# Optimization experiments

Measured on AMD Instinct MI355X. Metric: run time of the kernel, lower is better.

Reference implementation:

```python
import jax, jax.numpy as jnp
import numpy as np
import math

N = 12288
IN_MAIN, IN_MOD = 64, 128
NC_INNER, NC_QK, OUT_MAIN = 16, 8, 64

def setup_inputs() -> dict:
    key = jax.random.key(0)
    ks = jax.random.split(key, 8)
    s = lambda fan_in: 1.0 / np.sqrt(fan_in)
    return {
        "x_main": jax.random.normal(ks[0], (N, IN_MAIN), dtype=jnp.float32),
        "x_mod": jax.random.normal(ks[1], (N, IN_MOD), dtype=jnp.float32),
        "xyz": jax.random.uniform(ks[2], (N, 3), dtype=jnp.float32),
        # MLP E: [in_main+in_mod -> nc_inner -> nc_inner], bias=False (weights stored [in, out])
        "W_e1": jax.random.uniform(ks[3], (IN_MAIN + IN_MOD, NC_INNER), jnp.float32, -s(IN_MAIN + IN_MOD), s(IN_MAIN + IN_MOD)),
        "W_e2": jax.random.uniform(ks[4], (NC_INNER, NC_INNER), jnp.float32, -s(NC_INNER), s(NC_INNER)),
        "W_q": jax.random.uniform(ks[5], (NC_INNER, NC_QK), jnp.float32, -s(NC_INNER), s(NC_INNER)),
        "W_k": jax.random.uniform(ks[6], (NC_INNER, NC_QK), jnp.float32, -s(NC_INNER), s(NC_INNER)),
        "W_v": jax.random.uniform(ks[7], (NC_INNER, OUT_MAIN), jnp.float32, -s(NC_INNER), s(NC_INNER)),
    }

def reference(x_main, x_mod, xyz, W_e1, W_e2, W_q, W_k, W_v):
    # concat 3D + 2D features: [N, in_main+in_mod]
    x = jnp.concatenate((x_main, x_mod), axis=-1)
    # MLP E (bias-free Linear + ReLU per layer): [N, nc_inner]
    h = jax.nn.relu(jax.nn.relu(x @ W_e1) @ W_e2)
    Q = h @ W_q  # [N, nc_qk]
    K = h @ W_k  # [N, nc_qk]
    V = h @ W_v  # [N, out_main]
    scale = 1.0 / math.sqrt(NC_QK)
    scores = (Q @ K.T) * scale          # [N, N] full global attention
    attn = jax.nn.softmax(scores, axis=1)
    return attn @ V                     # [N, out_main]
```

## Files before the change

### kernel.cpp

```cpp
#include <hip/hip_runtime.h>
#include <stdint.h>


#define NN 12288

typedef float    f32x16 __attribute__((ext_vector_type(16)));
typedef short    s16x8  __attribute__((ext_vector_type(8)));
typedef unsigned short u16;

#define MFMA_32x32x16_BF16 __builtin_amdgcn_mfma_f32_32x32x16_bf16

#define OFF_QB   0u
#define OFF_VT   196608u
#define OFF_PO   2162688u

__device__ __forceinline__ float bf2f(u16 s) {
    union { unsigned int u; float f; } c; c.u = ((unsigned int)s) << 16; return c.f;
}
__device__ __forceinline__ u16 f2bf(float f) {
    union { float f; unsigned int u; } c; c.f = f;
    return (u16)((c.u + 0x8000u) >> 16);
}
__device__ __forceinline__ unsigned int pk2(float a, float b) {
    union { float f; unsigned int u; } ca, cb; ca.f = a; cb.f = b;
    return ((ca.u + 0x8000u) >> 16) | ((cb.u + 0x8000u) & 0xffff0000u);
}
__device__ __forceinline__ unsigned int pkbf(float a, float b) {
#if __has_builtin(__builtin_amdgcn_cvt_pk_bf16_f32)
    auto r = __builtin_amdgcn_cvt_pk_bf16_f32(a, b);
    union { decltype(r) v; unsigned int u; } c; c.v = r; return c.u;
#else
    return pk2(a, b);
#endif
}
__device__ __forceinline__ f32x16 zf16() {
    f32x16 z;
#pragma unroll
    for (int i = 0; i < 16; ++i) z[i] = 0.f;
    return z;
}
__device__ __forceinline__ s16x8 zs8() {
    s16x8 z;
#pragma unroll
    for (int i = 0; i < 8; ++i) z[i] = 0;
    return z;
}

union U8 { s16x8 v; unsigned int u[4]; };
union QV { uint4 q; s16x8 v; };

__global__ __launch_bounds__(256) void k1_qkv(
    const void* __restrict__ xmain, const void* __restrict__ xmod,
    const void* __restrict__ we1, const void* __restrict__ we2,
    const void* __restrict__ wqp, const void* __restrict__ wkp,
    const void* __restrict__ wvp,
    u16* __restrict__ qb, u16* __restrict__ vt)
{
    __shared__ float wf[4608];
    __shared__ int   sflag;
    __shared__ float lh1[64][4][17];
    __shared__ float lh2[64][17];

    const int t = threadIdx.x;
    const int r = t >> 2;
    const int p = t & 3;
    const int row = blockIdx.x * 64 + r;

    if (t == 0) sflag = 0;
    __syncthreads();
    {
        float v = bf2f(((const u16*)xmod)[2 * t]);
        if (fabsf(v) > 16.f) atomicAdd(&sflag, 1);
    }
    __syncthreads();
    const int isf32 = (sflag > 8);

    const float SCL = 0.51006979f;
    if (isf32) {
        const float* a1 = (const float*)we1; const float* a2 = (const float*)we2;
        const float* aq = (const float*)wqp; const float* ak = (const float*)wkp;
        const float* av = (const float*)wvp;
        for (int i = t; i < 4608; i += 256) {
            if      (i < 3072) wf[i] = a1[i];
            else if (i < 3328) wf[i] = a2[i - 3072];
            else if (i < 3456) wf[i] = aq[i - 3328] * SCL;
            else if (i < 3584) wf[i] = ak[i - 3456];
            else               wf[i] = av[i - 3584];
        }
    } else {
        const u16* a1 = (const u16*)we1; const u16* a2 = (const u16*)we2;
        const u16* aq = (const u16*)wqp; const u16* ak = (const u16*)wkp;
        const u16* av = (const u16*)wvp;
        for (int i = t; i < 4608; i += 256) {
            if      (i < 3072) wf[i] = bf2f(a1[i]);
            else if (i < 3328) wf[i] = bf2f(a2[i - 3072]);
            else if (i < 3456) wf[i] = bf2f(aq[i - 3328]) * SCL;
            else if (i < 3584) wf[i] = bf2f(ak[i - 3456]);
            else               wf[i] = bf2f(av[i - 3584]);
        }
    }
    __syncthreads();

    const float* __restrict__ W1 = wf;
    const float* __restrict__ W2 = wf + 3072;
    const float* __restrict__ Wq = wf + 3328;
    const float* __restrict__ Wk = wf + 3456;
    const float* __restrict__ Wv = wf + 3584;

    float h1p[16];
#pragma unroll
    for (int o = 0; o < 16; ++o) h1p[o] = 0.f;

    if (isf32) {
#pragma unroll
        for (int cc = 0; cc < 12; ++cc) {
            const int c = p + cc * 4;
            float4 xv = (c < 16)
                ? ((const float4*)xmain)[(size_t)row * 16 + c]
                : ((const float4*)xmod)[(size_t)row * 32 + (c - 16)];
            float xs[4] = {xv.x, xv.y, xv.z, xv.w};
#pragma unroll
            for (int j = 0; j < 4; ++j) {
                const float* wr = W1 + (c * 4 + j) * 16;
#pragma unroll
                for (int o = 0; o < 16; ++o) h1p[o] += xs[j] * wr[o];
            }
        }
    } else {
#pragma unroll
        for (int cc = 0; cc < 12; ++cc) {
            const int c = p + cc * 4;
            uint2 xv = (c < 16)
                ? ((const uint2*)xmain)[(size_t)row * 16 + c]
                : ((const uint2*)xmod)[(size_t)row * 32 + (c - 16)];
            float xs[4] = { bf2f((u16)(xv.x & 0xffff)), bf2f((u16)(xv.x >> 16)),
                            bf2f((u16)(xv.y & 0xffff)), bf2f((u16)(xv.y >> 16)) };
#pragma unroll
            for (int j = 0; j < 4; ++j) {
                const float* wr = W1 + (c * 4 + j) * 16;
#pragma unroll
                for (int o = 0; o < 16; ++o) h1p[o] += xs[j] * wr[o];
            }
        }
    }
#pragma unroll
    for (int o = 0; o < 16; ++o) lh1[r][p][o] = h1p[o];
    __syncthreads();

    float h1[16];
#pragma unroll
    for (int o = 0; o < 16; ++o)
        h1[o] = fmaxf(lh1[r][0][o] + lh1[r][1][o] + lh1[r][2][o] + lh1[r][3][o], 0.f);

#pragma unroll
    for (int oo = 0; oo < 4; ++oo) {
        const int o = p * 4 + oo;
        float s = 0.f;
#pragma unroll
        for (int j = 0; j < 16; ++j) s += h1[j] * W2[j * 16 + o];
        lh2[r][o] = fmaxf(s, 0.f);
    }
    __syncthreads();

    float h2[16];
#pragma unroll
    for (int j = 0; j < 16; ++j) h2[j] = lh2[r][j];

    {
        float q0 = 0.f, q1 = 0.f, k0 = 0.f, k1 = 0.f;
        const int o = 2 * p;
#pragma unroll
        for (int j = 0; j < 16; ++j) {
            q0 += h2[j] * Wq[j * 8 + o];
            q1 += h2[j] * Wq[j * 8 + o + 1];
            k0 += h2[j] * Wk[j * 8 + o];
            k1 += h2[j] * Wk[j * 8 + o + 1];
        }
        ((unsigned int*)qb)[(size_t)row * 4 + p] = pk2(q0, q1);
        ((unsigned int*)vt)[(size_t)(row >> 6) * 2304 + 2048 +
                            (row & 63) * 4 + p] = pk2(k0, k1);
    }

    {
        const int ch = row >> 6, tI = (row >> 5) & 1, kk = row & 31;
        const int b   = kk >> 4, kk4 = kk & 15;
        const int hh  = (kk4 >> 2) & 1;
        const int jj  = (kk4 & 3) + 4 * (kk4 >> 3);
        const size_t cbase = (size_t)ch * 4608 + (size_t)(tI * 4 + b) * 512
                           + hh * 256 + jj;
#pragma unroll
        for (int c16 = 0; c16 < 16; ++c16) {
            const int c = p * 16 + c16;
            float v = 0.f;
#pragma unroll
            for (int j = 0; j < 16; ++j) v += h2[j] * Wv[j * 64 + c];
            vt[cbase + (size_t)(c >> 5) * 1024 + (c & 31) * 8] = f2bf(v);
        }
    }
}


__global__ __launch_bounds__(256, 3) void k2_attn(
    const u16* __restrict__ qb, const u16* __restrict__ vt,
    u16* __restrict__ po, float* __restrict__ pl,
    int nsplit, int ntile)
{
    __shared__ float sf[4][2178];

    const int tid  = threadIdx.x;
    const int lane = tid & 63;
    const int half = lane >> 5;
    const int l31  = lane & 31;
    const int w    = tid >> 6;
    const int qB   = (blockIdx.x % 96) * 128;
    const int sp   = blockIdx.x / 96;
    const int myq  = qB + 32 * w;
    const int key_start = sp * (NN / nsplit);
    const char* vbase = (const char*)vt + (size_t)(key_start >> 6) * 9216;

    const f32x16 Z = zf16();
    s16x8 qf = zs8();
    if (!half) qf = *(const s16x8*)(qb + (size_t)(myq + l31) * 8);

    s16x8 ones;
#pragma unroll
    for (int i = 0; i < 8; ++i) ones[i] = (short)0x3F80;

    f32x16 acc0 = Z, acc1 = Z, accl = Z;

    QV kaA, f00A, f10A, f01A, f11A;
    QV kaB, f00B, f10B, f01B, f11B;

#define LDT(gt, ka, f00, f10, f01, f11) do {                                  \
    const char* cb_ = vbase + (size_t)((gt) >> 1) * 9216 + ((gt) & 1) * 4096; \
    (f00).q = *(const uint4*)(cb_ +        lane * 16);                        \
    (f01).q = *(const uint4*)(cb_ + 1024 + lane * 16);                        \
    (f10).q = *(const uint4*)(cb_ + 2048 + lane * 16);                        \
    (f11).q = *(const uint4*)(cb_ + 3072 + lane * 16);                        \
    (ka).q  = *(const uint4*)(vbase + (size_t)((gt) >> 1) * 9216 + 8192       \
                              + ((gt) & 1) * 512 + l31 * 16);                 \
} while (0)

#define TILE(ka, f00, f10, f01, f11) do {                                     \
    f32x16 S_ = MFMA_32x32x16_BF16((ka).v, qf, Z, 0, 0, 0);                   \
    float pr_[16];                                                            \
    _Pragma("unroll")                                                         \
    for (int r_ = 0; r_ < 16; ++r_) pr_[r_] = __builtin_amdgcn_exp2f(S_[r_]); \
    U8 p0_, p1_;                                                              \
    _Pragma("unroll")                                                         \
    for (int i_ = 0; i_ < 4; ++i_) {                                          \
        p0_.u[i_] = pkbf(pr_[2 * i_],     pr_[2 * i_ + 1]);                   \
        p1_.u[i_] = pkbf(pr_[8 + 2 * i_], pr_[8 + 2 * i_ + 1]);               \
    }                                                                         \
    accl = MFMA_32x32x16_BF16(ones, p0_.v, accl, 0, 0, 0);                    \
    accl = MFMA_32x32x16_BF16(ones, p1_.v, accl, 0, 0, 0);                    \
    acc0 = MFMA_32x32x16_BF16((f00).v, p0_.v, acc0, 0, 0, 0);                 \
    acc1 = MFMA_32x32x16_BF16((f10).v, p0_.v, acc1, 0, 0, 0);                 \
    acc0 = MFMA_32x32x16_BF16((f01).v, p1_.v, acc0, 0, 0, 0);                 \
    acc1 = MFMA_32x32x16_BF16((f11).v, p1_.v, acc1, 0, 0, 0);                 \
} while (0)

    LDT(0, kaA, f00A, f10A, f01A, f11A);
    int gt = 0;
    for (; gt + 2 < ntile; gt += 2) {
        LDT(gt + 1, kaB, f00B, f10B, f01B, f11B);
        TILE(kaA, f00A, f10A, f01A, f11A);
        LDT(gt + 2, kaA, f00A, f10A, f01A, f11A);
        TILE(kaB, f00B, f10B, f01B, f11B);
    }
    LDT(gt + 1, kaB, f00B, f10B, f01B, f11B);
    TILE(kaA, f00A, f10A, f01A, f11A);
    TILE(kaB, f00B, f10B, f01B, f11B);

#undef LDT
#undef TILE

    const float ls = accl[0];

    float* sfw = &sf[w][0];
#pragma unroll
    for (int r = 0; r < 16; ++r) {
        const int c = (r & 3) + 8 * (r >> 2) + 4 * half;
        sfw[c * 33 + l31]        = acc0[r];
        sfw[(32 + c) * 33 + l31] = acc1[r];
    }
    if (lane < 32) sfw[2112 + l31] = ls;

    u16* poS = po + (size_t)sp * (NN * 64);
    const int lq  = lane >> 1;
    const int cb0 = (lane & 1) * 32;
    unsigned int u[16];
#pragma unroll
    for (int i = 0; i < 16; ++i)
        u[i] = pkbf(sfw[(cb0 + 2 * i) * 33 + lq],
                    sfw[(cb0 + 2 * i + 1) * 33 + lq]);
    u16* dst = poS + (size_t)(myq + lq) * 64 + cb0;
    *(uint4*)(dst)      = make_uint4(u[0],  u[1],  u[2],  u[3]);
    *(uint4*)(dst + 8)  = make_uint4(u[4],  u[5],  u[6],  u[7]);
    *(uint4*)(dst + 16) = make_uint4(u[8],  u[9],  u[10], u[11]);
    *(uint4*)(dst + 24) = make_uint4(u[12], u[13], u[14], u[15]);
    if (lane < 32)
        pl[(size_t)sp * NN + myq + l31] = sfw[2112 + l31];
}

__global__ __launch_bounds__(256) void k3_norm(
    const u16* __restrict__ po, const float* __restrict__ pl,
    float4* __restrict__ out, int nsplit)
{
    const int i = blockIdx.x * 256 + threadIdx.x;
    const int row = i >> 4;
    const int c0 = (i & 15) * 4;
    float l = 0.f;
    float o0 = 0.f, o1 = 0.f, o2 = 0.f, o3 = 0.f;
    for (int s = 0; s < nsplit; ++s) {
        l += pl[(size_t)s * NN + row];
        uint2 p = *(const uint2*)(po + (size_t)s * (NN * 64) +
                                  (size_t)row * 64 + c0);
        o0 += bf2f((u16)(p.x & 0xffff)); o1 += bf2f((u16)(p.x >> 16));
        o2 += bf2f((u16)(p.y & 0xffff)); o3 += bf2f((u16)(p.y >> 16));
    }
    const float rl = 1.0f / l;
    out[i] = make_float4(o0 * rl, o1 * rl, o2 * rl, o3 * rl);
}

extern "C" void kernel_launch(void* const* d_in, const int* in_sizes, int n_in,
                              void* d_out, int out_size, void* d_ws, size_t ws_size,
                              hipStream_t stream)
{
    const void* xmain = d_in[0];
    const void* xmod  = d_in[1];
    const void* we1   = d_in[3];
    const void* we2   = d_in[4];
    const void* wq    = d_in[5];
    const void* wk    = d_in[6];
    const void* wv    = d_in[7];

    char* ws = (char*)d_ws;
    u16*   qb   = (u16*)  (ws + OFF_QB);
    u16*   vt   = (u16*)  (ws + OFF_VT);

    int S = 8;
    while (S > 1) {
        size_t need = (size_t)OFF_PO + (size_t)S * (NN * 64 * 2) +
                      (size_t)S * (NN * 4);
        if (ws_size >= need) break;
        S >>= 1;
    }
    u16*   po = (u16*)(ws + OFF_PO);
    float* pl = (float*)(ws + OFF_PO + (size_t)S * (NN * 64 * 2));
    const int ntile = NN / (32 * S);

    k1_qkv<<<192, 256, 0, stream>>>(xmain, xmod, we1, we2, wq, wk, wv,
                                    qb, vt);
    k2_attn<<<96 * S, 256, 0, stream>>>(qb, vt, po, pl, S, ntile);
    k3_norm<<<768, 256, 0, stream>>>(po, pl, (float4*)d_out, S);
}
```

Measured before the change: 127.1 us.

## Stage K/V tiles into LDS via async global_load_lds double buffering

```diff
diff --git a/kernel.cpp b/kernel.cpp
--- a/kernel.cpp
+++ b/kernel.cpp
@@ -13,6 +13,15 @@
 #define OFF_QB   0u
 #define OFF_VT   196608u
 #define OFF_PO   2162688u
+
+#define WC_VM(n)   (0x0F70 | (n))
+#define WC_LGKM0   (0xC07F)
+
+typedef __attribute__((address_space(3))) void lds_void_t;
+typedef const __attribute__((address_space(1))) void gbl_void_t;
+__device__ __forceinline__ void gld16(const void* g, void* l) {
+    __builtin_amdgcn_global_load_lds((gbl_void_t*)g, (lds_void_t*)l, 16, 0, 0);
+}
 
 __device__ __forceinline__ float bf2f(u16 s) {
     union { unsigned int u; float f; } c; c.u = ((unsigned int)s) << 16; return c.f;
@@ -166,6 +175,7 @@
 #pragma unroll
     for (int j = 0; j < 16; ++j) h2[j] = lh2[r][j];
 
+    const int tt = row >> 5, kk = row & 31;
     {
         float q0 = 0.f, q1 = 0.f, k0 = 0.f, k1 = 0.f;
         const int o = 2 * p;
@@ -177,17 +187,14 @@
             k1 += h2[j] * Wk[j * 8 + o + 1];
         }
         ((unsigned int*)qb)[(size_t)row * 4 + p] = pk2(q0, q1);
-        ((unsigned int*)vt)[(size_t)(row >> 6) * 2304 + 2048 +
-                            (row & 63) * 4 + p] = pk2(k0, k1);
+        ((unsigned int*)vt)[(size_t)tt * 1152 + 1024 + kk * 4 + p] = pk2(k0, k1);
     }
 
     {
-        const int ch = row >> 6, tI = (row >> 5) & 1, kk = row & 31;
         const int b   = kk >> 4, kk4 = kk & 15;
         const int hh  = (kk4 >> 2) & 1;
         const int jj  = (kk4 & 3) + 4 * (kk4 >> 3);
-        const size_t cbase = (size_t)ch * 4608 + (size_t)(tI * 4 + b) * 512
-                           + hh * 256 + jj;
+        const size_t cbase = (size_t)tt * 2304 + b * 512 + hh * 256 + jj;
 #pragma unroll
         for (int c16 = 0; c16 < 16; ++c16) {
             const int c = p * 16 + c16;
@@ -205,7 +212,7 @@
     u16* __restrict__ po, float* __restrict__ pl,
     int nsplit, int ntile)
 {
-    __shared__ float sf[4][2178];
+    __shared__ uint4 smem[2304];
 
     const int tid  = threadIdx.x;
     const int lane = tid & 63;
@@ -215,8 +222,10 @@
     const int qB   = (blockIdx.x % 96) * 128;
     const int sp   = blockIdx.x / 96;
     const int myq  = qB + 32 * w;
-    const int key_start = sp * (NN / nsplit);
-    const char* vbase = (const char*)vt + (size_t)(key_start >> 6) * 9216;
+    const int tile0 = sp * (NN / nsplit) / 32;
+
+    uint4* lb0 = &smem[w * 576];
+    uint4* lb1 = lb0 + 288;
 
     const f32x16 Z = zf16();
     s16x8 qf = zs8();
@@ -228,24 +237,24 @@
 
     f32x16 acc0 = Z, acc1 = Z, accl = Z;
 
-    QV kaA, f00A, f10A, f01A, f11A;
-    QV kaB, f00B, f10B, f01B, f11B;
-
-#define LDT(gt, ka, f00, f10, f01, f11) do {                                  \
-    const char* cb_ = vbase + (size_t)((gt) >> 1) * 9216 + ((gt) & 1) * 4096; \
-    (f00).q = *(const uint4*)(cb_ +        lane * 16);                        \
-    (f01).q = *(const uint4*)(cb_ + 1024 + lane * 16);                        \
-    (f10).q = *(const uint4*)(cb_ + 2048 + lane * 16);                        \
-    (f11).q = *(const uint4*)(cb_ + 3072 + lane * 16);                        \
-    (ka).q  = *(const uint4*)(vbase + (size_t)((gt) >> 1) * 9216 + 8192       \
-                              + ((gt) & 1) * 512 + l31 * 16);                 \
+#define STAGE(t, lbase) do {                                                  \
+    const char* g_ = (const char*)vt + (size_t)(t) * 4608 + lane * 16;        \
+    char* l_ = (char*)(lbase);                                                \
+    gld16(g_, l_);                                                            \
+    gld16(g_ + 1024, l_ + 1024);                                              \
+    gld16(g_ + 2048, l_ + 2048);                                              \
+    gld16(g_ + 3072, l_ + 3072);                                              \
+    if (lane < 32) gld16(g_ + 4096, l_ + 4096);                               \
 } while (0)
 
-#define TILE(ka, f00, f10, f01, f11) do {                                     \
-    f32x16 S_ = MFMA_32x32x16_BF16((ka).v, qf, Z, 0, 0, 0);                   \
+#define LDSK(lbase, ka) do {                                                  \
+    (ka).q = *((const uint4*)(lbase) + 256 + l31);                            \
+} while (0)
+
+#define FIN(S_, lbase) do {                                                   \
     float pr_[16];                                                            \
     _Pragma("unroll")                                                         \
-    for (int r_ = 0; r_ < 16; ++r_) pr_[r_] = __builtin_amdgcn_exp2f(S_[r_]); \
+    for (int r_ = 0; r_ < 16; ++r_) pr_[r_] = __builtin_amdgcn_exp2f((S_)[r_]);\
     U8 p0_, p1_;                                                              \
     _Pragma("unroll")                                                         \
     for (int i_ = 0; i_ < 4; ++i_) {                                          \
@@ -254,30 +263,66 @@
     }                                                                         \
     accl = MFMA_32x32x16_BF16(ones, p0_.v, accl, 0, 0, 0);                    \
     accl = MFMA_32x32x16_BF16(ones, p1_.v, accl, 0, 0, 0);                    \
-    acc0 = MFMA_32x32x16_BF16((f00).v, p0_.v, acc0, 0, 0, 0);                 \
-    acc1 = MFMA_32x32x16_BF16((f10).v, p0_.v, acc1, 0, 0, 0);                 \
-    acc0 = MFMA_32x32x16_BF16((f01).v, p1_.v, acc0, 0, 0, 0);                 \
-    acc1 = MFMA_32x32x16_BF16((f11).v, p1_.v, acc1, 0, 0, 0);                 \
+    QV f_;                                                                    \
+    f_.q = *((const uint4*)(lbase) + lane);                                   \
+    acc0 = MFMA_32x32x16_BF16(f_.v, p0_.v, acc0, 0, 0, 0);                    \
+    f_.q = *((const uint4*)(lbase) + 128 + lane);                             \
+    acc1 = MFMA_32x32x16_BF16(f_.v, p0_.v, acc1, 0, 0, 0);                    \
+    f_.q = *((const uint4*)(lbase) + 64 + lane);                              \
+    acc0 = MFMA_32x32x16_BF16(f_.v, p1_.v, acc0, 0, 0, 0);                    \
+    f_.q = *((const uint4*)(lbase) + 192 + lane);                             \
+    acc1 = MFMA_32x32x16_BF16(f_.v, p1_.v, acc1, 0, 0, 0);                    \
 } while (0)
 
-    LDT(0, kaA, f00A, f10A, f01A, f11A);
+#define WAIT_VM(n) do {                                                       \
+    __builtin_amdgcn_s_waitcnt(WC_VM(n));                                     \
+    __builtin_amdgcn_sched_barrier(0);                                        \
+} while (0)
+#define WAIT_LGKM() do {                                                      \
+    __builtin_amdgcn_s_waitcnt(WC_LGKM0);                                     \
+    __builtin_amdgcn_sched_barrier(0);                                        \
+} while (0)
+
+    STAGE(tile0 + 0, lb0);
+    STAGE(tile0 + 1, lb1);
+    WAIT_VM(5);
+    QV ka;
+    LDSK(lb0, ka);
+    f32x16 SA = MFMA_32x32x16_BF16(ka.v, qf, Z, 0, 0, 0);
+    f32x16 SB;
+
     int gt = 0;
     for (; gt + 2 < ntile; gt += 2) {
-        LDT(gt + 1, kaB, f00B, f10B, f01B, f11B);
-        TILE(kaA, f00A, f10A, f01A, f11A);
-        LDT(gt + 2, kaA, f00A, f10A, f01A, f11A);
-        TILE(kaB, f00B, f10B, f01B, f11B);
-    }
-    LDT(gt + 1, kaB, f00B, f10B, f01B, f11B);
-    TILE(kaA, f00A, f10A, f01A, f11A);
-    TILE(kaB, f00B, f10B, f01B, f11B);
-
-#undef LDT
-#undef TILE
+        WAIT_VM(0);
+        LDSK(lb1, ka);
+        SB = MFMA_32x32x16_BF16(ka.v, qf, Z, 0, 0, 0);
+        FIN(SA, lb0);
+        WAIT_LGKM();
+        STAGE(tile0 + gt + 2, lb0);
+        WAIT_VM(0);
+        LDSK(lb0, ka);
+        SA = MFMA_32x32x16_BF16(ka.v, qf, Z, 0, 0, 0);
+        FIN(SB, lb1);
+        WAIT_LGKM();
+        if (gt + 3 < ntile) STAGE(tile0 + gt + 3, lb1);
+    }
+    WAIT_VM(0);
+    LDSK(lb1, ka);
+    SB = MFMA_32x32x16_BF16(ka.v, qf, Z, 0, 0, 0);
+    FIN(SA, lb0);
+    FIN(SB, lb1);
+
+#undef STAGE
+#undef LDSK
+#undef FIN
+#undef WAIT_VM
+#undef WAIT_LGKM
 
     const float ls = accl[0];
 
-    float* sfw = &sf[w][0];
+    WAIT_LGKM_EPI:;
+    __builtin_amdgcn_s_waitcnt(WC_LGKM0);
+    float* sfw = (float*)&smem[w * 576];
 #pragma unroll
     for (int r = 0; r < 16; ++r) {
         const int c = (r & 3) + 8 * (r >> 2) + 4 * half;
```

Result: slower. 135.1 us (+6.3%).

## Use single-wave attention blocks, separate K buffer, VALU row sums, and more key splits

Applied to the files above, without the earlier changes.

```diff
diff --git a/kernel.cpp b/kernel.cpp
--- a/kernel.cpp
+++ b/kernel.cpp
@@ -11,7 +11,8 @@
 #define MFMA_32x32x16_BF16 __builtin_amdgcn_mfma_f32_32x32x16_bf16
 
 #define OFF_QB   0u
-#define OFF_VT   196608u
+#define OFF_KB   196608u
+#define OFF_VT   393216u
 #define OFF_PO   2162688u
 
 __device__ __forceinline__ float bf2f(u16 s) {
@@ -54,7 +55,7 @@
     const void* __restrict__ we1, const void* __restrict__ we2,
     const void* __restrict__ wqp, const void* __restrict__ wkp,
     const void* __restrict__ wvp,
-    u16* __restrict__ qb, u16* __restrict__ vt)
+    u16* __restrict__ qb, u16* __restrict__ kb, u16* __restrict__ vt)
 {
     __shared__ float wf[4608];
     __shared__ int   sflag;
@@ -166,6 +167,7 @@
 #pragma unroll
     for (int j = 0; j < 16; ++j) h2[j] = lh2[r][j];
 
+    const int tt = row >> 5, kk = row & 31;
     {
         float q0 = 0.f, q1 = 0.f, k0 = 0.f, k1 = 0.f;
         const int o = 2 * p;
@@ -177,17 +179,14 @@
             k1 += h2[j] * Wk[j * 8 + o + 1];
         }
         ((unsigned int*)qb)[(size_t)row * 4 + p] = pk2(q0, q1);
-        ((unsigned int*)vt)[(size_t)(row >> 6) * 2304 + 2048 +
-                            (row & 63) * 4 + p] = pk2(k0, k1);
+        ((unsigned int*)kb)[(size_t)row * 4 + p] = pk2(k0, k1);
     }
 
     {
-        const int ch = row >> 6, tI = (row >> 5) & 1, kk = row & 31;
         const int b   = kk >> 4, kk4 = kk & 15;
         const int hh  = (kk4 >> 2) & 1;
         const int jj  = (kk4 & 3) + 4 * (kk4 >> 3);
-        const size_t cbase = (size_t)ch * 4608 + (size_t)(tI * 4 + b) * 512
-                           + hh * 256 + jj;
+        const size_t cbase = (size_t)tt * 2048 + b * 512 + hh * 256 + jj;
 #pragma unroll
         for (int c16 = 0; c16 < 16; ++c16) {
             const int c = p * 16 + c16;
@@ -200,84 +199,85 @@
 }
 
 
-__global__ __launch_bounds__(256, 3) void k2_attn(
-    const u16* __restrict__ qb, const u16* __restrict__ vt,
+__global__ __launch_bounds__(64, 4) void k2_attn(
+    const u16* __restrict__ qb, const u16* __restrict__ kb,
+    const u16* __restrict__ vt,
     u16* __restrict__ po, float* __restrict__ pl,
     int nsplit, int ntile)
 {
-    __shared__ float sf[4][2178];
-
-    const int tid  = threadIdx.x;
-    const int lane = tid & 63;
+    __shared__ float sfw[2144];
+
+    const int lane = threadIdx.x & 63;
     const int half = lane >> 5;
     const int l31  = lane & 31;
-    const int w    = tid >> 6;
-    const int qB   = (blockIdx.x % 96) * 128;
-    const int sp   = blockIdx.x / 96;
-    const int myq  = qB + 32 * w;
-    const int key_start = sp * (NN / nsplit);
-    const char* vbase = (const char*)vt + (size_t)(key_start >> 6) * 9216;
+    const int qw   = blockIdx.x % 384;
+    const int sp   = blockIdx.x / 384;
+    const int myq  = qw * 32;
+    const int tile0 = sp * ntile;
 
     const f32x16 Z = zf16();
     s16x8 qf = zs8();
     if (!half) qf = *(const s16x8*)(qb + (size_t)(myq + l31) * 8);
 
-    s16x8 ones;
-#pragma unroll
-    for (int i = 0; i < 8; ++i) ones[i] = (short)0x3F80;
-
-    f32x16 acc0 = Z, acc1 = Z, accl = Z;
+    f32x16 acc0 = Z, acc1 = Z;
+    float ls0 = 0.f, ls1 = 0.f;
 
     QV kaA, f00A, f10A, f01A, f11A;
     QV kaB, f00B, f10B, f01B, f11B;
 
-#define LDT(gt, ka, f00, f10, f01, f11) do {                                  \
-    const char* cb_ = vbase + (size_t)((gt) >> 1) * 9216 + ((gt) & 1) * 4096; \
+#define LDT(t, ka, f00, f10, f01, f11) do {                                   \
+    const char* cb_ = (const char*)vt + (size_t)(tile0 + (t)) * 4096;         \
     (f00).q = *(const uint4*)(cb_ +        lane * 16);                        \
     (f01).q = *(const uint4*)(cb_ + 1024 + lane * 16);                        \
     (f10).q = *(const uint4*)(cb_ + 2048 + lane * 16);                        \
     (f11).q = *(const uint4*)(cb_ + 3072 + lane * 16);                        \
-    (ka).q  = *(const uint4*)(vbase + (size_t)((gt) >> 1) * 9216 + 8192       \
-                              + ((gt) & 1) * 512 + l31 * 16);                 \
+    (ka).q  = *(const uint4*)(kb + (size_t)((tile0 + (t)) * 32 + l31) * 8);   \
 } while (0)
 
 #define TILE(ka, f00, f10, f01, f11) do {                                     \
     f32x16 S_ = MFMA_32x32x16_BF16((ka).v, qf, Z, 0, 0, 0);                   \
-    float pr_[16];                                                            \
-    _Pragma("unroll")                                                         \
-    for (int r_ = 0; r_ < 16; ++r_) pr_[r_] = __builtin_amdgcn_exp2f(S_[r_]); \
+    float pr_[8];                                                             \
     U8 p0_, p1_;                                                              \
     _Pragma("unroll")                                                         \
-    for (int i_ = 0; i_ < 4; ++i_) {                                          \
-        p0_.u[i_] = pkbf(pr_[2 * i_],     pr_[2 * i_ + 1]);                   \
-        p1_.u[i_] = pkbf(pr_[8 + 2 * i_], pr_[8 + 2 * i_ + 1]);               \
+    for (int r_ = 0; r_ < 8; ++r_) {                                          \
+        pr_[r_] = __builtin_amdgcn_exp2f(S_[r_]);                             \
+        ls0 += pr_[r_];                                                       \
     }                                                                         \
-    accl = MFMA_32x32x16_BF16(ones, p0_.v, accl, 0, 0, 0);                    \
-    accl = MFMA_32x32x16_BF16(ones, p1_.v, accl, 0, 0, 0);                    \
+    _Pragma("unroll")                                                         \
+    for (int i_ = 0; i_ < 4; ++i_)                                            \
+        p0_.u[i_] = pkbf(pr_[2 * i_], pr_[2 * i_ + 1]);                       \
     acc0 = MFMA_32x32x16_BF16((f00).v, p0_.v, acc0, 0, 0, 0);                 \
     acc1 = MFMA_32x32x16_BF16((f10).v, p0_.v, acc1, 0, 0, 0);                 \
+    _Pragma("unroll")                                                         \
+    for (int r_ = 0; r_ < 8; ++r_) {                                          \
+        pr_[r_] = __builtin_amdgcn_exp2f(S_[r_ + 8]);                         \
+        ls1 += pr_[r_];                                                       \
+    }                                                                         \
+    _Pragma("unroll")                                                         \
+    for (int i_ = 0; i_ < 4; ++i_)                                            \
+        p1_.u[i_] = pkbf(pr_[2 * i_], pr_[2 * i_ + 1]);                       \
     acc0 = MFMA_32x32x16_BF16((f01).v, p1_.v, acc0, 0, 0, 0);                 \
     acc1 = MFMA_32x32x16_BF16((f11).v, p1_.v, acc1, 0, 0, 0);                 \
 } while (0)
 
     LDT(0, kaA, f00A, f10A, f01A, f11A);
+    LDT(1, kaB, f00B, f10B, f01B, f11B);
     int gt = 0;
     for (; gt + 2 < ntile; gt += 2) {
-        LDT(gt + 1, kaB, f00B, f10B, f01B, f11B);
         TILE(kaA, f00A, f10A, f01A, f11A);
         LDT(gt + 2, kaA, f00A, f10A, f01A, f11A);
         TILE(kaB, f00B, f10B, f01B, f11B);
-    }
-    LDT(gt + 1, kaB, f00B, f10B, f01B, f11B);
+        LDT(gt + 3, kaB, f00B, f10B, f01B, f11B);
+    }
     TILE(kaA, f00A, f10A, f01A, f11A);
     TILE(kaB, f00B, f10B, f01B, f11B);
 
 #undef LDT
 #undef TILE
 
-    const float ls = accl[0];
-
-    float* sfw = &sf[w][0];
+    float ls = ls0 + ls1;
+    ls += __shfl_xor(ls, 32, 64);
+
 #pragma unroll
     for (int r = 0; r < 16; ++r) {
         const int c = (r & 3) + 8 * (r >> 2) + 4 * half;
@@ -337,9 +337,10 @@
 
     char* ws = (char*)d_ws;
     u16*   qb   = (u16*)  (ws + OFF_QB);
+    u16*   kb   = (u16*)  (ws + OFF_KB);
     u16*   vt   = (u16*)  (ws + OFF_VT);
 
-    int S = 8;
+    int S = 16;
     while (S > 1) {
         size_t need = (size_t)OFF_PO + (size_t)S * (NN * 64 * 2) +
                       (size_t)S * (NN * 4);
@@ -351,7 +352,7 @@
     const int ntile = NN / (32 * S);
 
     k1_qkv<<<192, 256, 0, stream>>>(xmain, xmod, we1, we2, wq, wk, wv,
-                                    qb, vt);
-    k2_attn<<<96 * S, 256, 0, stream>>>(qb, vt, po, pl, S, ntile);
+                                    qb, kb, vt);
+    k2_attn<<<384 * S, 64, 0, stream>>>(qb, kb, vt, po, pl, S, ntile);
     k3_norm<<<768, 256, 0, stream>>>(po, pl, (float4*)d_out, S);
 }
```

After: 251.4 us. +97.8%, slower.
